# Kernel tuning notes

Hardware: AMD Instinct MI355X
Metric: run time of the kernel (lower is better)

## Reference

```python
import jax, jax.numpy as jnp
import numpy as np

N_NODES = 50000
N_EDGES = 800000
NODE_F = 5
EDGE_F = 4
HID = 128


def _glorot(key, shape):
    fan_in, fan_out = shape[0], shape[1]
    lim = float(np.sqrt(6.0 / (fan_in + fan_out)))
    return jax.random.uniform(key, shape, jnp.float32, -lim, lim)


def setup_inputs() -> dict:
    key = jax.random.key(0)
    ks = jax.random.split(key, 12)
    x = jax.random.normal(ks[0], (N_NODES, NODE_F), jnp.float32)
    edge_attr = jax.random.normal(ks[1], (N_EDGES, EDGE_F), jnp.float32)
    edge_index = jax.random.randint(ks[2], (2, N_EDGES), 0, N_NODES, jnp.int64)
    return {
        "x": x,
        "edge_attr": edge_attr,
        "W1": _glorot(ks[3], (NODE_F, HID)),
        "b1": jnp.zeros((HID,), jnp.float32),
        "W2": _glorot(ks[4], (HID, HID)),
        "b2": jnp.zeros((HID,), jnp.float32),
        "Wm1": _glorot(ks[5], (2 * HID + EDGE_F, HID)),
        "bm1": jnp.zeros((HID,), jnp.float32),
        "Wm2": _glorot(ks[6], (HID, 1)),
        "bm2": jnp.zeros((1,), jnp.float32),
        "edge_index": edge_index,
    }


def _gcn_conv(x, W, b, row, col, norm, n_nodes):
    # GCNConv: out = D^{-1/2} (A + I) D^{-1/2} X W + b
    xw = x @ W                                   # [N, H]
    msg = norm[:, None] * xw[row]                # [E+N, H] gather + scale
    agg = jax.ops.segment_sum(msg, col, num_segments=n_nodes)
    return agg + b


def reference(x, edge_attr, W1, b1, W2, b2, Wm1, bm1, Wm2, bm2, edge_index):
    n = x.shape[0]
    src, dst = edge_index[0], edge_index[1]
    # add self-loops (PyG GCNConv default)
    loop = jnp.arange(n, dtype=edge_index.dtype)
    row = jnp.concatenate([src, loop])
    col = jnp.concatenate([dst, loop])
    # symmetric normalization, in-degree w/ self-loops
    deg = jax.ops.segment_sum(jnp.ones_like(col, dtype=x.dtype), col, num_segments=n)
    dis = jnp.where(deg > 0, jax.lax.rsqrt(deg), 0.0)
    norm = dis[row] * dis[col]

    h = jax.nn.relu(_gcn_conv(x, W1, b1, row, col, norm, n))
    h = _gcn_conv(h, W2, b2, row, col, norm, n)

    # gather-concat edge MLP
    edge_emb = jnp.concatenate([h[src], h[dst], edge_attr], axis=1)  # [E, 2H+F]
    out = jax.nn.relu(edge_emb @ Wm1 + bm1) @ Wm2 + bm2              # [E, 1]
    return jax.nn.sigmoid(out[:, 0])
```

## Files before the change

### kernel.cpp

```cpp
#include <hip/hip_runtime.h>
#include <math.h>

#define HID 128
typedef unsigned int uint;
typedef __attribute__((ext_vector_type(8))) __bf16 bf16x8;
typedef __attribute__((ext_vector_type(4))) float f32x4;
typedef __attribute__((ext_vector_type(2))) float f32x2;


__device__ __forceinline__ uint pack_bf2(float x, float y) {
    union { float f; uint u; } a, b;
    a.f = x; b.f = y;
    uint lo = (a.u + 0x7fffu + ((a.u >> 16) & 1u)) >> 16;
    uint hi = (b.u + 0x7fffu + ((b.u >> 16) & 1u)) & 0xffff0000u;
    return lo | hi;
}

__device__ __forceinline__ unsigned short bf16r(float x) {
    union { float f; uint u; } a; a.f = x;
    return (unsigned short)((a.u + 0x7fffu + ((a.u >> 16) & 1u)) >> 16);
}

__device__ __forceinline__ f32x2 bf2f(uint v) {
    union { uint u[2]; f32x2 f; } r;
    r.u[0] = v << 16;
    r.u[1] = v & 0xffff0000u;
    return r.f;
}

__device__ __forceinline__ f32x2 mk2(float s) { f32x2 r; r.x = s; r.y = s; return r; }
__device__ __forceinline__ f32x2 max2z(f32x2 a) {
    f32x2 r; r.x = fmaxf(a.x, 0.f); r.y = fmaxf(a.y, 0.f); return r;
}
__device__ __forceinline__ f32x2 shfl_xor2(f32x2 v, int m) {
    f32x2 r; r.x = __shfl_xor(v.x, m, 64); r.y = __shfl_xor(v.y, m, 64); return r;
}


__global__ void zero_prep(int* __restrict__ cnt, int N,
                          const float* __restrict__ W2, const float* __restrict__ Wm1,
                          const float* __restrict__ b2, const float* __restrict__ bm1,
                          uint* __restrict__ fWc, float* __restrict__ brow,
                          float* __restrict__ zbias) {
    int stride = gridDim.x * blockDim.x;
    int t0 = blockIdx.x * blockDim.x + threadIdx.x;
    for (int i = t0; i < N; i += stride) cnt[i] = 0;
    if (t0 < 128) zbias[t0] = 0.f;
    for (int i = t0; i < 16384; i += stride) {
        int p = i & 3, lane = (i >> 2) & 63, kk = (i >> 8) & 3, ct = i >> 10;
        int k = kk * 32 + (lane >> 4) * 8 + p * 2;
        int n2 = ct * 16 + (lane & 15);
        const float* wmc = (n2 < 128) ? (Wm1 + n2) : (Wm1 + 128 * HID + (n2 - 128));
        const float* w2r0 = W2 + (size_t)k * HID;
        const float* w2r1 = w2r0 + HID;
        float d0 = 0.f, d1 = 0.f;
        for (int j = 0; j < HID; ++j) {
            float wm = wmc[(size_t)j * HID];
            d0 += w2r0[j] * wm;
            d1 += w2r1[j] * wm;
        }
        fWc[i] = pack_bf2(d0, d1);
    }
    for (int i = t0; i < 256; i += stride) {
        const float* wmc = (i < 128) ? (Wm1 + i) : (Wm1 + 128 * HID + (i - 128));
        float d = 0.f;
        for (int j = 0; j < HID; ++j) d += b2[j] * wmc[(size_t)j * HID];
        brow[i] = d + ((i < 128) ? bm1[i] : 0.f);
    }
}

__global__ void hist_rank(const int* __restrict__ dst, int* __restrict__ cnt,
                          int* __restrict__ rank, int E) {
    int e = blockIdx.x * blockDim.x + threadIdx.x;
    if (e < E) rank[e] = atomicAdd(&cnt[dst[e]], 1);
}

__global__ void scan1(const int* __restrict__ cnt, int* __restrict__ excl,
                      int* __restrict__ bsum, int N) {
    __shared__ int sh[256];
    int tid = threadIdx.x;
    int gid = blockIdx.x * 256 + tid;
    int v = (gid < N) ? cnt[gid] : 0;
    sh[tid] = v;
    __syncthreads();
    for (int o = 1; o < 256; o <<= 1) {
        int t = (tid >= o) ? sh[tid - o] : 0;
        __syncthreads();
        sh[tid] += t;
        __syncthreads();
    }
    if (gid < N) excl[gid] = sh[tid] - v;
    if (tid == 255) bsum[blockIdx.x] = sh[255];
}

__global__ void scan3x(const int* __restrict__ cnt, int* __restrict__ rowptr,
                       const int* __restrict__ bsum,
                       float* __restrict__ dis, const float* __restrict__ x,
                       float* __restrict__ xps, int N, int E, int NB) {
    __shared__ int sh[256];
    __shared__ int ex[256];
    int tid = threadIdx.x;
    int v = (tid < NB) ? bsum[tid] : 0;
    sh[tid] = v;
    __syncthreads();
    for (int o = 1; o < 256; o <<= 1) {
        int t = (tid >= o) ? sh[tid - o] : 0;
        __syncthreads();
        sh[tid] += t;
        __syncthreads();
    }
    ex[tid] = sh[tid] - v;
    __syncthreads();
    int gid = blockIdx.x * 256 + tid;
    if (gid < N) {
        rowptr[gid] = rowptr[gid] + ex[blockIdx.x];
        float dn = rsqrtf((float)cnt[gid] + 1.0f);
        dis[gid] = dn;
        const float* xr = x + (size_t)gid * 5;
        float* xo = xps + (size_t)gid * 8;
        *(float4*)xo = make_float4(dn * xr[0], dn * xr[1], dn * xr[2], dn * xr[3]);
        xo[4] = dn * xr[4];
    }
    if (gid == N) rowptr[N] = E;
}

__global__ void scatter2(const int* __restrict__ src, const int* __restrict__ dst,
                         const int* __restrict__ rowptr, const int* __restrict__ rank,
                         uint2* __restrict__ csr2, int E) {
    int e = blockIdx.x * blockDim.x + threadIdx.x;
    if (e < E) {
        int d = dst[e];
        int pos = rowptr[d] + rank[e];
        csr2[pos] = make_uint2((uint)src[e] | ((uint)d << 16), (uint)e);
    }
}


__global__ void aggx_kernel(const float* __restrict__ xps, const uint2* __restrict__ csr2,
                            const int* __restrict__ rowptr, const float* __restrict__ dis,
                            float* __restrict__ sx, int N) {
    int n = blockIdx.x * blockDim.x + threadIdx.x;
    if (n >= N) return;
    int beg = rowptr[n], end = rowptr[n + 1];
    float a0 = 0.f, a1 = 0.f, a2 = 0.f, a3 = 0.f, a4 = 0.f;
    for (int i = beg; i < end; ++i) {
        int s = (int)(csr2[i].x & 0xffffu);
        float4 v = *(const float4*)(xps + (size_t)s * 8);
        float v4 = xps[(size_t)s * 8 + 4];
        a0 += v.x; a1 += v.y; a2 += v.z; a3 += v.w; a4 += v4;
    }
    float4 v = *(const float4*)(xps + (size_t)n * 8);
    float v4 = xps[(size_t)n * 8 + 4];
    a0 += v.x; a1 += v.y; a2 += v.z; a3 += v.w; a4 += v4;
    float dn = dis[n];
    float* o = sx + (size_t)n * 8;
    *(float4*)o = make_float4(dn * a0, dn * a1, dn * a2, dn * a3);
    o[4] = dn * a4;
}

__global__ void hs1_kernel(const float* __restrict__ sx, const float* __restrict__ W1,
                           const float* __restrict__ b1, const float* __restrict__ dis,
                           uint* __restrict__ hs1, int N) {
    int idx = blockIdx.x * blockDim.x + threadIdx.x;
    if (idx >= N * 64) return;
    int n = idx >> 6, p = idx & 63;
    int j = p * 2;
    const float* sr = sx + (size_t)n * 8;
    float a0 = b1[j], a1 = b1[j + 1];
    #pragma unroll
    for (int k = 0; k < 5; ++k) {
        float s = sr[k];
        a0 += s * W1[k * HID + j];
        a1 += s * W1[k * HID + j + 1];
    }
    float dn = dis[n];
    a0 = fmaxf(a0, 0.f) * dn;
    a1 = fmaxf(a1, 0.f) * dn;
    hs1[idx] = pack_bf2(a0, a1);
}


__global__ void aggregate_kernel(const uint4* __restrict__ xws, const uint2* __restrict__ csr2,
                                 const int* __restrict__ rowptr, const float* __restrict__ dis,
                                 const float* __restrict__ bias, uint4* __restrict__ out,
                                 int N, int do_relu) {
    int wave = threadIdx.x >> 6;
    int lane = threadIdx.x & 63;
    int n = blockIdx.x * (blockDim.x >> 6) + wave;
    if (n >= N) return;
    int gl = lane & 15, grp = lane >> 4;
    int beg = rowptr[n], end = rowptr[n + 1];

    f32x2 acc[4];
    #pragma unroll
    for (int p = 0; p < 4; ++p) acc[p] = mk2(0.f);

    for (int base = beg + grp; base < end; base += 16) {
        int i1 = base + 4, i2 = base + 8, i3 = base + 12;
        int s0 = (int)(csr2[base].x & 0xffffu);
        int s1 = (int)(csr2[(i1 < end) ? i1 : beg].x & 0xffffu);
        int s2 = (int)(csr2[(i2 < end) ? i2 : beg].x & 0xffffu);
        int s3 = (int)(csr2[(i3 < end) ? i3 : beg].x & 0xffffu);
        uint4 v0 = xws[(size_t)s0 * 16 + gl];
        uint4 v1 = xws[(size_t)s1 * 16 + gl];
        uint4 v2 = xws[(size_t)s2 * 16 + gl];
        uint4 v3 = xws[(size_t)s3 * 16 + gl];
        f32x2 w1 = mk2((i1 < end) ? 1.f : 0.f);
        f32x2 w2 = mk2((i2 < end) ? 1.f : 0.f);
        f32x2 w3 = mk2((i3 < end) ? 1.f : 0.f);
        acc[0] += bf2f(v0.x);  acc[1] += bf2f(v0.y);
        acc[2] += bf2f(v0.z);  acc[3] += bf2f(v0.w);
        acc[0] += bf2f(v1.x) * w1;  acc[1] += bf2f(v1.y) * w1;
        acc[2] += bf2f(v1.z) * w1;  acc[3] += bf2f(v1.w) * w1;
        acc[0] += bf2f(v2.x) * w2;  acc[1] += bf2f(v2.y) * w2;
        acc[2] += bf2f(v2.z) * w2;  acc[3] += bf2f(v2.w) * w2;
        acc[0] += bf2f(v3.x) * w3;  acc[1] += bf2f(v3.y) * w3;
        acc[2] += bf2f(v3.z) * w3;  acc[3] += bf2f(v3.w) * w3;
    }
    #pragma unroll
    for (int p = 0; p < 4; ++p) {
        acc[p] += shfl_xor2(acc[p], 16);
        acc[p] += shfl_xor2(acc[p], 32);
    }

    if (grp == 0) {
        uint4 sv = xws[(size_t)n * 16 + gl];
        f32x2 dn = mk2(dis[n]);
        const float* bp = bias + gl * 8;
        f32x2 o[4];
        o[0] = (acc[0] + bf2f(sv.x)) * dn + *(const f32x2*)(bp);
        o[1] = (acc[1] + bf2f(sv.y)) * dn + *(const f32x2*)(bp + 2);
        o[2] = (acc[2] + bf2f(sv.z)) * dn + *(const f32x2*)(bp + 4);
        o[3] = (acc[3] + bf2f(sv.w)) * dn + *(const f32x2*)(bp + 6);
        if (do_relu) {
            #pragma unroll
            for (int p = 0; p < 4; ++p) o[p] = max2z(o[p]);
        }
        uint4 pk;
        pk.x = pack_bf2(o[0].x, o[0].y);
        pk.y = pack_bf2(o[1].x, o[1].y);
        pk.z = pack_bf2(o[2].x, o[2].y);
        pk.w = pack_bf2(o[3].x, o[3].y);
        out[(size_t)n * 16 + gl] = pk;
    }
}

__launch_bounds__(256)
__global__ void mfma_gemm(const uint4* __restrict__ A, const uint4* __restrict__ Bf,
                          const float* __restrict__ bias, const float* __restrict__ rowscale,
                          unsigned short* __restrict__ out, int N, int CT, int bias_ct) {
    int wave = threadIdx.x >> 6, lane = threadIdx.x & 63;
    int rbase = (blockIdx.x * 4 + wave) * 16;
    if (rbase >= N) return;
    int quad = lane >> 4, gl = lane & 15;
    int r = rbase + gl;
    if (r >= N) r = N - 1;

    bf16x8 afr[4];
    #pragma unroll
    for (int kk = 0; kk < 4; ++kk)
        afr[kk] = *(const bf16x8*)&A[(size_t)r * 16 + kk * 4 + quad];

    float rs[4];
    #pragma unroll
    for (int reg = 0; reg < 4; ++reg) {
        int row = rbase + quad * 4 + reg;
        rs[reg] = (rowscale && row < N) ? rowscale[row] : 1.f;
    }

    int ncols = CT * 16;
    for (int c = 0; c < CT; ++c) {
        f32x4 acc = {0.f, 0.f, 0.f, 0.f};
        #pragma unroll
        for (int kk = 0; kk < 4; ++kk) {
            bf16x8 bfr = *(const bf16x8*)&Bf[(size_t)(c * 4 + kk) * 64 + lane];
            acc = __builtin_amdgcn_mfma_f32_16x16x32_bf16(afr[kk], bfr, acc, 0, 0, 0);
        }
        float bv = (c < bias_ct) ? bias[c * 16 + gl] : 0.f;
        #pragma unroll
        for (int reg = 0; reg < 4; ++reg) {
            int row = rbase + quad * 4 + reg;
            if (row < N)
                out[(size_t)row * ncols + c * 16 + gl] = bf16r((acc[reg] + bv) * rs[reg]);
        }
    }
}

__launch_bounds__(256)
__global__ void edge_mlp_kernel(const uint4* __restrict__ HsHd, const float4* __restrict__ ea,
                                const uint2* __restrict__ csr2,
                                const float* __restrict__ Wb, const float* __restrict__ Wm2,
                                const float* __restrict__ bm2,
                                float* __restrict__ out, int E) {
    int lane = threadIdx.x & 63;
    int gl = lane & 15, grp = lane >> 4;

    f32x2 wb[4][4], w2[4];
    #pragma unroll
    for (int k = 0; k < 4; ++k) {
        const f32x2* wp = (const f32x2*)(Wb + k * HID + gl * 8);
        #pragma unroll
        for (int p = 0; p < 4; ++p) wb[k][p] = wp[p];
    }
    {
        const f32x2* wp = (const f32x2*)(Wm2 + gl * 8);
        #pragma unroll
        for (int p = 0; p < 4; ++p) w2[p] = wp[p];
    }
    float b2v = bm2[0];

    int gwave = (blockIdx.x * blockDim.x + threadIdx.x) >> 6;
    int nw = (gridDim.x * blockDim.x) >> 6;
    for (int base = gwave * 8; base < E; base += nw * 8) {
        int i0 = base + grp;
        int i1 = i0 + 4;
        int j0 = (i0 < E) ? i0 : (E - 1);
        int j1 = (i1 < E) ? i1 : (E - 1);
        uint2 ce0 = csr2[j0];
        uint2 ce1 = csr2[j1];
        int s0i = (int)(ce0.x & 0xffffu), d0i = (int)(ce0.x >> 16);
        int s1i = (int)(ce1.x & 0xffffu), d1i = (int)(ce1.x >> 16);
        uint4 hv0 = HsHd[(size_t)s0i * 32 + gl];
        uint4 dv0 = HsHd[(size_t)d0i * 32 + 16 + gl];
        uint4 hv1 = HsHd[(size_t)s1i * 32 + gl];
        uint4 dv1 = HsHd[(size_t)d1i * 32 + 16 + gl];
        float4 ea0 = ea[ce0.y];
        float4 ea1 = ea[ce1.y];

        uint hu0[4] = {hv0.x, hv0.y, hv0.z, hv0.w};
        uint du0[4] = {dv0.x, dv0.y, dv0.z, dv0.w};
        uint hu1[4] = {hv1.x, hv1.y, hv1.z, hv1.w};
        uint du1[4] = {dv1.x, dv1.y, dv1.z, dv1.w};

        f32x2 p20 = mk2(0.f), p21 = mk2(0.f);
        f32x2 a0 = mk2(ea0.x), b0 = mk2(ea0.y), c0 = mk2(ea0.z), d0 = mk2(ea0.w);
        f32x2 a1 = mk2(ea1.x), b1 = mk2(ea1.y), c1 = mk2(ea1.z), d1 = mk2(ea1.w);
        #pragma unroll
        for (int p = 0; p < 4; ++p) {
            f32x2 t0 = bf2f(hu0[p]) + bf2f(du0[p]);
            t0 += a0 * wb[0][p];
            t0 += b0 * wb[1][p];
            t0 += c0 * wb[2][p];
            t0 += d0 * wb[3][p];
            t0 = max2z(t0);
            p20 += t0 * w2[p];
            f32x2 t1 = bf2f(hu1[p]) + bf2f(du1[p]);
            t1 += a1 * wb[0][p];
            t1 += b1 * wb[1][p];
            t1 += c1 * wb[2][p];
            t1 += d1 * wb[3][p];
            t1 = max2z(t1);
            p21 += t1 * w2[p];
        }
        float p0 = p20.x + p20.y;
        float p1 = p21.x + p21.y;
        p0 += __shfl_xor(p0, 1, 64);   p1 += __shfl_xor(p1, 1, 64);
        p0 += __shfl_xor(p0, 2, 64);   p1 += __shfl_xor(p1, 2, 64);
        p0 += __shfl_xor(p0, 4, 64);   p1 += __shfl_xor(p1, 4, 64);
        p0 += __shfl_xor(p0, 8, 64);   p1 += __shfl_xor(p1, 8, 64);
        if (gl == 0 && i0 < E) out[ce0.y] = 1.f / (1.f + expf(-(p0 + b2v)));
        if (gl == 0 && i1 < E) out[ce1.y] = 1.f / (1.f + expf(-(p1 + b2v)));
    }
}


extern "C" void kernel_launch(void* const* d_in, const int* in_sizes, int n_in,
                              void* d_out, int out_size, void* d_ws, size_t ws_size,
                              hipStream_t stream) {
    const float* x    = (const float*)d_in[0];
    const float* ea   = (const float*)d_in[1];
    const float* W1   = (const float*)d_in[2];
    const float* b1   = (const float*)d_in[3];
    const float* W2   = (const float*)d_in[4];
    const float* b2   = (const float*)d_in[5];
    const float* Wm1  = (const float*)d_in[6];
    const float* bm1  = (const float*)d_in[7];
    const float* Wm2  = (const float*)d_in[8];
    const float* bm2  = (const float*)d_in[9];
    const int*   ei   = (const int*)d_in[10];

    const int N = in_sizes[0] / 5;
    const int E = in_sizes[1] / 4;
    const int* src = ei;
    const int* dst = ei + E;
    float* out = (float*)d_out;

    char* ws = (char*)d_ws;
    size_t off = 0;
    auto alloc = [&](size_t bytes) -> void* {
        void* p = ws + off;
        off = (off + bytes + 255) & ~(size_t)255;
        return p;
    };
    int*    cnt    = (int*)alloc((size_t)N * 4);
    int*    rowptr = (int*)alloc((size_t)(N + 1) * 4);
    int*    bsum   = (int*)alloc(256 * 4);
    float*  dis    = (float*)alloc((size_t)N * 4);
    int*    rank   = (int*)alloc((size_t)(E + 8) * 4);
    uint2*  csr2   = (uint2*)alloc((size_t)(E + 8) * 8);
    float*  xps    = (float*)alloc((size_t)N * 8 * 4);
    float*  sx     = (float*)alloc((size_t)N * 8 * 4);
    uint*   R      = (uint*)alloc((size_t)N * 128 * 4);
    uint*   g      = (uint*)alloc((size_t)N * 64 * 4);
    uint*   fWc    = (uint*)alloc(16384 * 4);
    float*  brow   = (float*)alloc(256 * 4);
    float*  zbias  = (float*)alloc(128 * 4);
    (void)ws_size; (void)n_in; (void)out_size;

    uint* hs1  = R;
    uint* HsHd = R;

    const int NB = (N + 255) / 256;
    const int EB = (E + 255) / 256;

    zero_prep<<<NB, 256, 0, stream>>>(cnt, N, W2, Wm1, b2, bm1, fWc, brow, zbias);
    hist_rank<<<EB, 256, 0, stream>>>(dst, cnt, rank, E);
    scan1<<<NB, 256, 0, stream>>>(cnt, rowptr, bsum, N);
    scan3x<<<NB, 256, 0, stream>>>(cnt, rowptr, bsum, dis, x, xps, N, E, NB);
    scatter2<<<EB, 256, 0, stream>>>(src, dst, rowptr, rank, csr2, E);

    aggx_kernel<<<NB, 256, 0, stream>>>(xps, csr2, rowptr, dis, sx, N);
    hs1_kernel<<<(N * 64 + 255) / 256, 256, 0, stream>>>(sx, W1, b1, dis, hs1, N);

    aggregate_kernel<<<(N + 3) / 4, 256, 0, stream>>>((const uint4*)hs1, csr2, rowptr, dis,
                                                      zbias, (uint4*)g, N, 0);

    mfma_gemm<<<(N + 63) / 64, 256, 0, stream>>>((const uint4*)g, (const uint4*)fWc,
                                                 brow, nullptr,
                                                 (unsigned short*)HsHd, N, 16, 16);

    edge_mlp_kernel<<<2048, 256, 0, stream>>>((const uint4*)HsHd, (const float4*)ea, csr2,
                                              Wm1 + 256 * HID, Wm2, bm2, out, E);
}
```

Measured before the change: 284.9 us.

## Fuse layer-1 aggregation with W1 projection, and layer-2 aggregation with MFMA GEMM

Merges the 5-wide feature aggregation with the W1 projection, ReLU and bf16 pack into one kernel, with W1 and b1 staged in shared memory. Merges the 128-wide neighbour aggregation with the MFMA GEMM: each block aggregates 16 nodes into an LDS tile, then runs the MFMA on that tile. This removes the sx and g intermediate buffers, their global round trips and two launches. The edge MLP now handles four edges per 16-lane group to raise memory-level parallelism. The trade-offs are that each layer-1 thread writes a full 256-byte row, so stores are poorly coalesced, and hs1 and HsHd now need separate buffers.

Measured after the change: 265.4 us. -6.8%, faster.

```diff
diff --git a/kernel.cpp b/kernel.cpp
--- a/kernel.cpp
+++ b/kernel.cpp
@@ -40,12 +40,10 @@
 __global__ void zero_prep(int* __restrict__ cnt, int N,
                           const float* __restrict__ W2, const float* __restrict__ Wm1,
                           const float* __restrict__ b2, const float* __restrict__ bm1,
-                          uint* __restrict__ fWc, float* __restrict__ brow,
-                          float* __restrict__ zbias) {
+                          uint* __restrict__ fWc, float* __restrict__ brow) {
     int stride = gridDim.x * blockDim.x;
     int t0 = blockIdx.x * blockDim.x + threadIdx.x;
     for (int i = t0; i < N; i += stride) cnt[i] = 0;
-    if (t0 < 128) zbias[t0] = 0.f;
     for (int i = t0; i < 16384; i += stride) {
         int p = i & 3, lane = (i >> 2) & 63, kk = (i >> 8) & 3, ct = i >> 10;
         int k = kk * 32 + (lane >> 4) * 8 + p * 2;
@@ -135,11 +133,19 @@
     }
 }
 
-
-__global__ void aggx_kernel(const float* __restrict__ xps, const uint2* __restrict__ csr2,
-                            const int* __restrict__ rowptr, const float* __restrict__ dis,
-                            float* __restrict__ sx, int N) {
-    int n = blockIdx.x * blockDim.x + threadIdx.x;
+__launch_bounds__(256)
+__global__ void layer1_kernel(const float* __restrict__ xps, const uint2* __restrict__ csr2,
+                              const int* __restrict__ rowptr, const float* __restrict__ dis,
+                              const float* __restrict__ W1, const float* __restrict__ b1,
+                              uint* __restrict__ hs1, int N) {
+    __shared__ float sW[5 * HID];
+    __shared__ float sb[HID];
+    int tid = threadIdx.x;
+    for (int i = tid; i < 5 * HID; i += 256) sW[i] = W1[i];
+    for (int i = tid; i < HID; i += 256) sb[i] = b1[i];
+    __syncthreads();
+
+    int n = blockIdx.x * 256 + tid;
     if (n >= N) return;
     int beg = rowptr[n], end = rowptr[n + 1];
     float a0 = 0.f, a1 = 0.f, a2 = 0.f, a3 = 0.f, a4 = 0.f;
@@ -149,139 +155,110 @@
         float v4 = xps[(size_t)s * 8 + 4];
         a0 += v.x; a1 += v.y; a2 += v.z; a3 += v.w; a4 += v4;
     }
-    float4 v = *(const float4*)(xps + (size_t)n * 8);
-    float v4 = xps[(size_t)n * 8 + 4];
-    a0 += v.x; a1 += v.y; a2 += v.z; a3 += v.w; a4 += v4;
+    {
+        float4 v = *(const float4*)(xps + (size_t)n * 8);
+        float v4 = xps[(size_t)n * 8 + 4];
+        a0 += v.x; a1 += v.y; a2 += v.z; a3 += v.w; a4 += v4;
+    }
     float dn = dis[n];
-    float* o = sx + (size_t)n * 8;
-    *(float4*)o = make_float4(dn * a0, dn * a1, dn * a2, dn * a3);
-    o[4] = dn * a4;
-}
-
-__global__ void hs1_kernel(const float* __restrict__ sx, const float* __restrict__ W1,
-                           const float* __restrict__ b1, const float* __restrict__ dis,
-                           uint* __restrict__ hs1, int N) {
-    int idx = blockIdx.x * blockDim.x + threadIdx.x;
-    if (idx >= N * 64) return;
-    int n = idx >> 6, p = idx & 63;
-    int j = p * 2;
-    const float* sr = sx + (size_t)n * 8;
-    float a0 = b1[j], a1 = b1[j + 1];
-    #pragma unroll
-    for (int k = 0; k < 5; ++k) {
-        float s = sr[k];
-        a0 += s * W1[k * HID + j];
-        a1 += s * W1[k * HID + j + 1];
-    }
-    float dn = dis[n];
-    a0 = fmaxf(a0, 0.f) * dn;
-    a1 = fmaxf(a1, 0.f) * dn;
-    hs1[idx] = pack_bf2(a0, a1);
-}
-
-
-__global__ void aggregate_kernel(const uint4* __restrict__ xws, const uint2* __restrict__ csr2,
-                                 const int* __restrict__ rowptr, const float* __restrict__ dis,
-                                 const float* __restrict__ bias, uint4* __restrict__ out,
-                                 int N, int do_relu) {
-    int wave = threadIdx.x >> 6;
-    int lane = threadIdx.x & 63;
-    int n = blockIdx.x * (blockDim.x >> 6) + wave;
-    if (n >= N) return;
+    a0 *= dn; a1 *= dn; a2 *= dn; a3 *= dn; a4 *= dn;
+
+    uint* op = hs1 + (size_t)n * 64;
+    #pragma unroll 4
+    for (int p = 0; p < 64; ++p) {
+        int j = p * 2;
+        float t0 = sb[j]     + a0 * sW[j]     + a1 * sW[HID + j]     + a2 * sW[2*HID + j]
+                             + a3 * sW[3*HID + j] + a4 * sW[4*HID + j];
+        float t1 = sb[j + 1] + a0 * sW[j + 1] + a1 * sW[HID + j + 1] + a2 * sW[2*HID + j + 1]
+                             + a3 * sW[3*HID + j + 1] + a4 * sW[4*HID + j + 1];
+        op[p] = pack_bf2(fmaxf(t0, 0.f) * dn, fmaxf(t1, 0.f) * dn);
+    }
+}
+
+__launch_bounds__(256)
+__global__ void agg_gemm(const uint4* __restrict__ hs1, const uint2* __restrict__ csr2,
+                         const int* __restrict__ rowptr, const float* __restrict__ dis,
+                         const uint4* __restrict__ Bf, const float* __restrict__ brow,
+                         unsigned short* __restrict__ out, int N) {
+    __shared__ uint gt[16][64];
+    int wave = threadIdx.x >> 6, lane = threadIdx.x & 63;
     int gl = lane & 15, grp = lane >> 4;
-    int beg = rowptr[n], end = rowptr[n + 1];
-
-    f32x2 acc[4];
-    #pragma unroll
-    for (int p = 0; p < 4; ++p) acc[p] = mk2(0.f);
-
-    for (int base = beg + grp; base < end; base += 16) {
-        int i1 = base + 4, i2 = base + 8, i3 = base + 12;
-        int s0 = (int)(csr2[base].x & 0xffffu);
-        int s1 = (int)(csr2[(i1 < end) ? i1 : beg].x & 0xffffu);
-        int s2 = (int)(csr2[(i2 < end) ? i2 : beg].x & 0xffffu);
-        int s3 = (int)(csr2[(i3 < end) ? i3 : beg].x & 0xffffu);
-        uint4 v0 = xws[(size_t)s0 * 16 + gl];
-        uint4 v1 = xws[(size_t)s1 * 16 + gl];
-        uint4 v2 = xws[(size_t)s2 * 16 + gl];
-        uint4 v3 = xws[(size_t)s3 * 16 + gl];
-        f32x2 w1 = mk2((i1 < end) ? 1.f : 0.f);
-        f32x2 w2 = mk2((i2 < end) ? 1.f : 0.f);
-        f32x2 w3 = mk2((i3 < end) ? 1.f : 0.f);
-        acc[0] += bf2f(v0.x);  acc[1] += bf2f(v0.y);
-        acc[2] += bf2f(v0.z);  acc[3] += bf2f(v0.w);
-        acc[0] += bf2f(v1.x) * w1;  acc[1] += bf2f(v1.y) * w1;
-        acc[2] += bf2f(v1.z) * w1;  acc[3] += bf2f(v1.w) * w1;
-        acc[0] += bf2f(v2.x) * w2;  acc[1] += bf2f(v2.y) * w2;
-        acc[2] += bf2f(v2.z) * w2;  acc[3] += bf2f(v2.w) * w2;
-        acc[0] += bf2f(v3.x) * w3;  acc[1] += bf2f(v3.y) * w3;
-        acc[2] += bf2f(v3.z) * w3;  acc[3] += bf2f(v3.w) * w3;
-    }
-    #pragma unroll
-    for (int p = 0; p < 4; ++p) {
-        acc[p] += shfl_xor2(acc[p], 16);
-        acc[p] += shfl_xor2(acc[p], 32);
-    }
-
-    if (grp == 0) {
-        uint4 sv = xws[(size_t)n * 16 + gl];
-        f32x2 dn = mk2(dis[n]);
-        const float* bp = bias + gl * 8;
-        f32x2 o[4];
-        o[0] = (acc[0] + bf2f(sv.x)) * dn + *(const f32x2*)(bp);
-        o[1] = (acc[1] + bf2f(sv.y)) * dn + *(const f32x2*)(bp + 2);
-        o[2] = (acc[2] + bf2f(sv.z)) * dn + *(const f32x2*)(bp + 4);
-        o[3] = (acc[3] + bf2f(sv.w)) * dn + *(const f32x2*)(bp + 6);
-        if (do_relu) {
-            #pragma unroll
-            for (int p = 0; p < 4; ++p) o[p] = max2z(o[p]);
-        }
-        uint4 pk;
-        pk.x = pack_bf2(o[0].x, o[0].y);
-        pk.y = pack_bf2(o[1].x, o[1].y);
-        pk.z = pack_bf2(o[2].x, o[2].y);
-        pk.w = pack_bf2(o[3].x, o[3].y);
-        out[(size_t)n * 16 + gl] = pk;
-    }
-}
-
-__launch_bounds__(256)
-__global__ void mfma_gemm(const uint4* __restrict__ A, const uint4* __restrict__ Bf,
-                          const float* __restrict__ bias, const float* __restrict__ rowscale,
-                          unsigned short* __restrict__ out, int N, int CT, int bias_ct) {
-    int wave = threadIdx.x >> 6, lane = threadIdx.x & 63;
-    int rbase = (blockIdx.x * 4 + wave) * 16;
-    if (rbase >= N) return;
-    int quad = lane >> 4, gl = lane & 15;
-    int r = rbase + gl;
-    if (r >= N) r = N - 1;
-
+    int nb = blockIdx.x * 16;
+
+    for (int q = 0; q < 4; ++q) {
+        int r = wave * 4 + q;
+        int n = nb + r;
+        if (n < N) {
+            int beg = rowptr[n], end = rowptr[n + 1];
+            f32x2 acc[4];
+            #pragma unroll
+            for (int p = 0; p < 4; ++p) acc[p] = mk2(0.f);
+            for (int base = beg + grp; base < end; base += 16) {
+                int i1 = base + 4, i2 = base + 8, i3 = base + 12;
+                int s0 = (int)(csr2[base].x & 0xffffu);
+                int s1 = (int)(csr2[(i1 < end) ? i1 : beg].x & 0xffffu);
+                int s2 = (int)(csr2[(i2 < end) ? i2 : beg].x & 0xffffu);
+                int s3 = (int)(csr2[(i3 < end) ? i3 : beg].x & 0xffffu);
+                uint4 v0 = hs1[(size_t)s0 * 16 + gl];
+                uint4 v1 = hs1[(size_t)s1 * 16 + gl];
+                uint4 v2 = hs1[(size_t)s2 * 16 + gl];
+                uint4 v3 = hs1[(size_t)s3 * 16 + gl];
+                f32x2 w1 = mk2((i1 < end) ? 1.f : 0.f);
+                f32x2 w2 = mk2((i2 < end) ? 1.f : 0.f);
+                f32x2 w3 = mk2((i3 < end) ? 1.f : 0.f);
+                acc[0] += bf2f(v0.x);  acc[1] += bf2f(v0.y);
+                acc[2] += bf2f(v0.z);  acc[3] += bf2f(v0.w);
+                acc[0] += bf2f(v1.x) * w1;  acc[1] += bf2f(v1.y) * w1;
+                acc[2] += bf2f(v1.z) * w1;  acc[3] += bf2f(v1.w) * w1;
+                acc[0] += bf2f(v2.x) * w2;  acc[1] += bf2f(v2.y) * w2;
+                acc[2] += bf2f(v2.z) * w2;  acc[3] += bf2f(v2.w) * w2;
+                acc[0] += bf2f(v3.x) * w3;  acc[1] += bf2f(v3.y) * w3;
+                acc[2] += bf2f(v3.z) * w3;  acc[3] += bf2f(v3.w) * w3;
+            }
+            #pragma unroll
+            for (int p = 0; p < 4; ++p) {
+                acc[p] += shfl_xor2(acc[p], 16);
+                acc[p] += shfl_xor2(acc[p], 32);
+            }
+            if (grp == 0) {
+                uint4 sv = hs1[(size_t)n * 16 + gl];
+                f32x2 dn = mk2(dis[n]);
+                f32x2 o0 = (acc[0] + bf2f(sv.x)) * dn;
+                f32x2 o1 = (acc[1] + bf2f(sv.y)) * dn;
+                f32x2 o2 = (acc[2] + bf2f(sv.z)) * dn;
+                f32x2 o3 = (acc[3] + bf2f(sv.w)) * dn;
+                gt[r][gl * 4]     = pack_bf2(o0.x, o0.y);
+                gt[r][gl * 4 + 1] = pack_bf2(o1.x, o1.y);
+                gt[r][gl * 4 + 2] = pack_bf2(o2.x, o2.y);
+                gt[r][gl * 4 + 3] = pack_bf2(o3.x, o3.y);
+            }
+        } else if (grp == 0) {
+            gt[r][gl * 4] = 0; gt[r][gl * 4 + 1] = 0;
+            gt[r][gl * 4 + 2] = 0; gt[r][gl * 4 + 3] = 0;
+        }
+    }
+    __syncthreads();
+
+    int quad = lane >> 4;
     bf16x8 afr[4];
     #pragma unroll
     for (int kk = 0; kk < 4; ++kk)
-        afr[kk] = *(const bf16x8*)&A[(size_t)r * 16 + kk * 4 + quad];
-
-    float rs[4];
-    #pragma unroll
-    for (int reg = 0; reg < 4; ++reg) {
-        int row = rbase + quad * 4 + reg;
-        rs[reg] = (rowscale && row < N) ? rowscale[row] : 1.f;
-    }
-
-    int ncols = CT * 16;
-    for (int c = 0; c < CT; ++c) {
+        afr[kk] = *(const bf16x8*)&gt[gl][kk * 16 + quad * 4];
+
+    for (int cc = 0; cc < 4; ++cc) {
+        int c = wave * 4 + cc;
         f32x4 acc = {0.f, 0.f, 0.f, 0.f};
         #pragma unroll
         for (int kk = 0; kk < 4; ++kk) {
             bf16x8 bfr = *(const bf16x8*)&Bf[(size_t)(c * 4 + kk) * 64 + lane];
             acc = __builtin_amdgcn_mfma_f32_16x16x32_bf16(afr[kk], bfr, acc, 0, 0, 0);
         }
-        float bv = (c < bias_ct) ? bias[c * 16 + gl] : 0.f;
+        float bv = brow[c * 16 + gl];
         #pragma unroll
         for (int reg = 0; reg < 4; ++reg) {
-            int row = rbase + quad * 4 + reg;
+            int row = nb + quad * 4 + reg;
             if (row < N)
-                out[(size_t)row * ncols + c * 16 + gl] = bf16r((acc[reg] + bv) * rs[reg]);
+                out[(size_t)row * 256 + c * 16 + gl] = bf16r(acc[reg] + bv);
         }
     }
 }
@@ -311,55 +288,52 @@
 
     int gwave = (blockIdx.x * blockDim.x + threadIdx.x) >> 6;
     int nw = (gridDim.x * blockDim.x) >> 6;
-    for (int base = gwave * 8; base < E; base += nw * 8) {
-        int i0 = base + grp;
-        int i1 = i0 + 4;
-        int j0 = (i0 < E) ? i0 : (E - 1);
-        int j1 = (i1 < E) ? i1 : (E - 1);
-        uint2 ce0 = csr2[j0];
-        uint2 ce1 = csr2[j1];
-        int s0i = (int)(ce0.x & 0xffffu), d0i = (int)(ce0.x >> 16);
-        int s1i = (int)(ce1.x & 0xffffu), d1i = (int)(ce1.x >> 16);
-        uint4 hv0 = HsHd[(size_t)s0i * 32 + gl];
-        uint4 dv0 = HsHd[(size_t)d0i * 32 + 16 + gl];
-        uint4 hv1 = HsHd[(size_t)s1i * 32 + gl];
-        uint4 dv1 = HsHd[(size_t)d1i * 32 + 16 + gl];
-        float4 ea0 = ea[ce0.y];
-        float4 ea1 = ea[ce1.y];
-
-        uint hu0[4] = {hv0.x, hv0.y, hv0.z, hv0.w};
-        uint du0[4] = {dv0.x, dv0.y, dv0.z, dv0.w};
-        uint hu1[4] = {hv1.x, hv1.y, hv1.z, hv1.w};
-        uint du1[4] = {dv1.x, dv1.y, dv1.z, dv1.w};
-
-        f32x2 p20 = mk2(0.f), p21 = mk2(0.f);
-        f32x2 a0 = mk2(ea0.x), b0 = mk2(ea0.y), c0 = mk2(ea0.z), d0 = mk2(ea0.w);
-        f32x2 a1 = mk2(ea1.x), b1 = mk2(ea1.y), c1 = mk2(ea1.z), d1 = mk2(ea1.w);
-        #pragma unroll
-        for (int p = 0; p < 4; ++p) {
-            f32x2 t0 = bf2f(hu0[p]) + bf2f(du0[p]);
-            t0 += a0 * wb[0][p];
-            t0 += b0 * wb[1][p];
-            t0 += c0 * wb[2][p];
-            t0 += d0 * wb[3][p];
-            t0 = max2z(t0);
-            p20 += t0 * w2[p];
-            f32x2 t1 = bf2f(hu1[p]) + bf2f(du1[p]);
-            t1 += a1 * wb[0][p];
-            t1 += b1 * wb[1][p];
-            t1 += c1 * wb[2][p];
-            t1 += d1 * wb[3][p];
-            t1 = max2z(t1);
-            p21 += t1 * w2[p];
-        }
-        float p0 = p20.x + p20.y;
-        float p1 = p21.x + p21.y;
-        p0 += __shfl_xor(p0, 1, 64);   p1 += __shfl_xor(p1, 1, 64);
-        p0 += __shfl_xor(p0, 2, 64);   p1 += __shfl_xor(p1, 2, 64);
-        p0 += __shfl_xor(p0, 4, 64);   p1 += __shfl_xor(p1, 4, 64);
-        p0 += __shfl_xor(p0, 8, 64);   p1 += __shfl_xor(p1, 8, 64);
-        if (gl == 0 && i0 < E) out[ce0.y] = 1.f / (1.f + expf(-(p0 + b2v)));
-        if (gl == 0 && i1 < E) out[ce1.y] = 1.f / (1.f + expf(-(p1 + b2v)));
+    for (int base = gwave * 16; base < E; base += nw * 16) {
+        int i0 = base + grp * 4;
+        uint2 ce[4];
+        uint4 hv[4], dv[4];
+        float4 eav[4];
+        #pragma unroll
+        for (int t = 0; t < 4; ++t) {
+            int i = i0 + t;
+            int j = (i < E) ? i : (E - 1);
+            ce[t] = csr2[j];
+            hv[t] = HsHd[(size_t)(ce[t].x & 0xffffu) * 32 + gl];
+            dv[t] = HsHd[(size_t)(ce[t].x >> 16) * 32 + 16 + gl];
+            eav[t] = ea[ce[t].y];
+        }
+        float pr[4];
+        #pragma unroll
+        for (int t = 0; t < 4; ++t) {
+            uint hu[4] = {hv[t].x, hv[t].y, hv[t].z, hv[t].w};
+            uint du[4] = {dv[t].x, dv[t].y, dv[t].z, dv[t].w};
+            f32x2 e0 = mk2(eav[t].x), e1 = mk2(eav[t].y);
+            f32x2 e2 = mk2(eav[t].z), e3 = mk2(eav[t].w);
+            f32x2 p2 = mk2(0.f);
+            #pragma unroll
+            for (int p = 0; p < 4; ++p) {
+                f32x2 tt = bf2f(hu[p]) + bf2f(du[p]);
+                tt += e0 * wb[0][p];
+                tt += e1 * wb[1][p];
+                tt += e2 * wb[2][p];
+                tt += e3 * wb[3][p];
+                tt = max2z(tt);
+                p2 += tt * w2[p];
+            }
+            pr[t] = p2.x + p2.y;
+        }
+        #pragma unroll
+        for (int o = 1; o <= 8; o <<= 1) {
+            #pragma unroll
+            for (int t = 0; t < 4; ++t) pr[t] += __shfl_xor(pr[t], o, 64);
+        }
+        if (gl == 0) {
+            #pragma unroll
+            for (int t = 0; t < 4; ++t) {
+                int i = i0 + t;
+                if (i < E) out[ce[t].y] = 1.f / (1.f + expf(-(pr[t] + b2v)));
+            }
+        }
     }
 }
 
@@ -399,35 +373,26 @@
     int*    rank   = (int*)alloc((size_t)(E + 8) * 4);
     uint2*  csr2   = (uint2*)alloc((size_t)(E + 8) * 8);
     float*  xps    = (float*)alloc((size_t)N * 8 * 4);
-    float*  sx     = (float*)alloc((size_t)N * 8 * 4);
-    uint*   R      = (uint*)alloc((size_t)N * 128 * 4);
-    uint*   g      = (uint*)alloc((size_t)N * 64 * 4);
+    uint*   hs1    = (uint*)alloc((size_t)N * 64 * 4);
+    uint*   HsHd   = (uint*)alloc((size_t)N * 128 * 4);
     uint*   fWc    = (uint*)alloc(16384 * 4);
     float*  brow   = (float*)alloc(256 * 4);
-    float*  zbias  = (float*)alloc(128 * 4);
     (void)ws_size; (void)n_in; (void)out_size;
-
-    uint* hs1  = R;
-    uint* HsHd = R;
 
     const int NB = (N + 255) / 256;
     const int EB = (E + 255) / 256;
 
-    zero_prep<<<NB, 256, 0, stream>>>(cnt, N, W2, Wm1, b2, bm1, fWc, brow, zbias);
+    zero_prep<<<NB, 256, 0, stream>>>(cnt, N, W2, Wm1, b2, bm1, fWc, brow);
     hist_rank<<<EB, 256, 0, stream>>>(dst, cnt, rank, E);
     scan1<<<NB, 256, 0, stream>>>(cnt, rowptr, bsum, N);
     scan3x<<<NB, 256, 0, stream>>>(cnt, rowptr, bsum, dis, x, xps, N, E, NB);
     scatter2<<<EB, 256, 0, stream>>>(src, dst, rowptr, rank, csr2, E);
 
-    aggx_kernel<<<NB, 256, 0, stream>>>(xps, csr2, rowptr, dis, sx, N);
-    hs1_kernel<<<(N * 64 + 255) / 256, 256, 0, stream>>>(sx, W1, b1, dis, hs1, N);
-
-    aggregate_kernel<<<(N + 3) / 4, 256, 0, stream>>>((const uint4*)hs1, csr2, rowptr, dis,
-                                                      zbias, (uint4*)g, N, 0);
-
-    mfma_gemm<<<(N + 63) / 64, 256, 0, stream>>>((const uint4*)g, (const uint4*)fWc,
-                                                 brow, nullptr,
-                                                 (unsigned short*)HsHd, N, 16, 16);
+    layer1_kernel<<<NB, 256, 0, stream>>>(xps, csr2, rowptr, dis, W1, b1, hs1, N);
+
+    agg_gemm<<<(N + 15) / 16, 256, 0, stream>>>((const uint4*)hs1, csr2, rowptr, dis,
+                                                (const uint4*)fWc, brow,
+                                                (unsigned short*)HsHd, N);
 
     edge_mlp_kernel<<<2048, 256, 0, stream>>>((const uint4*)HsHd, (const float4*)ea, csr2,
                                               Wm1 + 256 * HID, Wm2, bm2, out, E);
```
